# Kernel optimization log

Hardware: AMD Instinct MI355X
Metric: run time of the kernel (lower is better)

The kernel has to match this reference:

```python
import jax, jax.numpy as jnp
import numpy as np

N, E, B = 8192, 131072, 256
F_ATOM, D, H, HD, L, FC, BINS = 92, 256, 8, 32, 6, 512, 256
VMIN, VMAX = 0.0, 8.0


def layer_norm(x, g, b, eps=1e-5):
    mu = jnp.mean(x, axis=-1, keepdims=True)
    var = jnp.var(x, axis=-1, keepdims=True)
    return (x - mu) * jax.lax.rsqrt(var + eps) * g + b


def silu(x):
    return x * jax.nn.sigmoid(x)


def setup_inputs() -> dict:
    key = jax.random.key(0)
    ks = iter(jax.random.split(key, 80))

    def lin(fan_in, shape):
        return jax.random.normal(next(ks), shape, jnp.float32) / np.sqrt(fan_in)

    inp = {
        'x': jax.random.normal(next(ks), (N, F_ATOM), jnp.float32),
        'edge_attr': jax.random.normal(next(ks), (E, 3), jnp.float32) * 2.0,
        'edge_index': jax.random.randint(next(ks), (2, E), 0, N, dtype=jnp.int32),
        'batch': jnp.sort(jax.random.randint(next(ks), (N,), 0, B, dtype=jnp.int32)),
        # atom_embedding: Linear(92,256) -> LN -> SiLU -> Linear(256,256)
        'aw1': lin(F_ATOM, (F_ATOM, D)), 'ab1': jnp.zeros((D,)),
        'ag1': jnp.ones((D,)), 'abt1': jnp.zeros((D,)),
        'aw2': lin(D, (D, D)), 'ab2': jnp.zeros((D,)),
        # rbf MLP: Linear(256,256) LN SiLU Linear LN SiLU Linear
        'rw1': lin(BINS, (BINS, D)), 'rb1': jnp.zeros((D,)),
        'rg1': jnp.ones((D,)), 'rbt1': jnp.zeros((D,)),
        'rw2': lin(D, (D, D)), 'rb2': jnp.zeros((D,)),
        'rg2': jnp.ones((D,)), 'rbt2': jnp.zeros((D,)),
        'rw3': lin(D, (D, D)), 'rb3': jnp.zeros((D,)),
        # L stacked PrdnetConv (edge-conditioned multi-head graph attention)
        'Wq': lin(D, (L, D, D)), 'bq': jnp.zeros((L, D)),
        'Wk': lin(D, (L, D, D)), 'bk': jnp.zeros((L, D)),
        'Wv': lin(D, (L, D, D)), 'bv': jnp.zeros((L, D)),
        'We': lin(D, (L, D, D)), 'be': jnp.zeros((L, D)),
        'Wo': lin(D, (L, D, D)), 'bo': jnp.zeros((L, D)),
        'lng': jnp.ones((L, D)), 'lnb': jnp.zeros((L, D)),
        # FC head: Linear(256,512) then fc_out Linear(512,1)
        'fw1': lin(D, (D, FC)), 'fb1': jnp.zeros((FC,)),
        'fow': lin(FC, (FC, 1)), 'fob': jnp.zeros((1,)),
    }
    return inp


def _forward(x, edge_attr, edge_index, batch, aw1, ab1, ag1, abt1, aw2, ab2,
             rw1, rb1, rg1, rbt1, rw2, rb2, rg2, rbt2, rw3, rb3,
             Wq, bq, Wk, bk, Wv, bv, We, be, Wo, bo, lng, lnb,
             fw1, fb1, fow, fob):
    # atom embedding (dropout = identity at inference)
    node = silu(layer_norm(x @ aw1 + ab1, ag1, abt1)) @ aw2 + ab2  # [N, D]

    # RBF expansion of edge lengths, then edge MLP
    d = jnp.linalg.norm(edge_attr, axis=1)  # [E]
    centers = jnp.linspace(VMIN, VMAX, BINS)
    gamma = 1.0 / (centers[1] - centers[0]) ** 2
    rbf = jnp.exp(-gamma * (d[:, None] - centers[None, :]) ** 2)  # [E, BINS]
    e = silu(layer_norm(rbf @ rw1 + rb1, rg1, rbt1))
    e = silu(layer_norm(e @ rw2 + rb2, rg2, rbt2))
    e = e @ rw3 + rb3  # [E, D]

    src, dst = edge_index[0], edge_index[1]
    inv_sqrt = 1.0 / np.sqrt(HD)
    for l in range(L):
        res = node
        q = (node @ Wq[l] + bq[l]).reshape(N, H, HD)
        k = (node @ Wk[l] + bk[l]).reshape(N, H, HD)
        v = (node @ Wv[l] + bv[l]).reshape(N, H, HD)
        ee = (e @ We[l] + be[l]).reshape(E, H, HD)
        kj = k[src] + ee  # edge-conditioned keys [E, H, HD]
        vj = v[src] + ee  # edge-conditioned values
        score = jnp.sum(q[dst] * kj, axis=-1) * inv_sqrt  # [E, H]
        smax = jax.ops.segment_max(score, dst, num_segments=N)  # [N, H]
        ex = jnp.exp(score - smax[dst])
        den = jax.ops.segment_sum(ex, dst, num_segments=N)
        alpha = ex / (den[dst] + 1e-16)  # neighborhood softmax [E, H]
        msg = jax.ops.segment_sum(alpha[:, :, None] * vj, dst, num_segments=N)
        out = msg.reshape(N, D) @ Wo[l] + bo[l]
        out = layer_norm(out, lng[l], lnb[l])
        node = out + res  # residual

    # scatter-mean graph pooling
    sums = jax.ops.segment_sum(node, batch, num_segments=B)  # [B, D]
    cnt = jax.ops.segment_sum(jnp.ones((N,), node.dtype), batch, num_segments=B)
    feats = sums / jnp.clip(cnt, 1.0)[:, None]

    feats = feats @ fw1 + fb1  # single fc layer: no act (i == len-1 in source)
    return feats @ fow + fob  # [B, 1], identity link


def reference(x, edge_attr, edge_index, batch, aw1, ab1, ag1, abt1, aw2, ab2,
              rw1, rb1, rg1, rbt1, rw2, rb2, rg2, rbt2, rw3, rb3,
              Wq, bq, Wk, bk, Wv, bv, We, be, Wo, bo, lng, lnb,
              fw1, fb1, fow, fob):
    return _forward(x, edge_attr, edge_index, batch, aw1, ab1, ag1, abt1, aw2,
                    ab2, rw1, rb1, rg1, rbt1, rw2, rb2, rg2, rbt2, rw3, rb3,
                    Wq, bq, Wk, bk, Wv, bv, We, be, Wo, bo, lng, lnb,
                    fw1, fb1, fow, fob)
```

## Files before the change

### kernel.cpp

```cpp
#include <hip/hip_runtime.h>
#include <hip/hip_bf16.h>
#include <cstddef>

#define NN    8192
#define EE    131072
#define BB    256
#define F_AT  92
#define DD    256
#define HH    8
#define HDIM  32
#define LL    6
#define FCD   512

typedef __hip_bfloat16 bf16;
typedef __attribute__((ext_vector_type(8))) __bf16 bf16x8;
typedef __attribute__((ext_vector_type(4))) float f32x4;

__device__ __forceinline__ float to_f(float x) { return x; }
__device__ __forceinline__ float to_f(bf16 x) { return __bfloat162float(x); }
__device__ __forceinline__ float bfu(unsigned short u) {
    return __uint_as_float(((unsigned)u) << 16);
}
__device__ __forceinline__ unsigned short bfbits(float x) {
    bf16 h = __float2bfloat16(x);
    return *(unsigned short*)&h;
}
__device__ __forceinline__ void store_v(float* p, float v) { *p = v; }
__device__ __forceinline__ void store_v(bf16* p, float v) { *p = __float2bfloat16(v); }

__device__ __forceinline__ float4 load4(const float* p) { return *(const float4*)p; }
__device__ __forceinline__ float4 load4(const bf16* p) {
    const ushort4 r = *(const ushort4*)p;
    return make_float4(bfu(r.x), bfu(r.y), bfu(r.z), bfu(r.w));
}

__device__ __forceinline__ void store_f4(float* p, const float4& f) {
    *(float4*)p = f;
}
__device__ __forceinline__ void store_f4(bf16* p, const float4& f) {
    ushort4 u = {bfbits(f.x), bfbits(f.y), bfbits(f.z), bfbits(f.w)};
    *(ushort4*)p = u;
}

__device__ __forceinline__ bf16x8 ld8(const bf16* p) { return *(const bf16x8*)p; }
__device__ __forceinline__ bf16x8 ld8(const float* p) {
    const float4 f0 = *(const float4*)p;
    const float4 f1 = *(const float4*)(p + 4);
    bf16x8 r;
    r[0] = (__bf16)f0.x; r[1] = (__bf16)f0.y; r[2] = (__bf16)f0.z; r[3] = (__bf16)f0.w;
    r[4] = (__bf16)f1.x; r[5] = (__bf16)f1.y; r[6] = (__bf16)f1.z; r[7] = (__bf16)f1.w;
    return r;
}

__device__ __forceinline__ void async_copy16(const void* g, void* l) {
    __builtin_amdgcn_global_load_lds(
        (const __attribute__((address_space(1))) unsigned int*)g,
        (__attribute__((address_space(3))) unsigned int*)l, 16, 0, 0);
}

__global__ __launch_bounds__(256) void transpose_weights(
    const float* __restrict__ rw1, const float* __restrict__ rw2,
    const float* __restrict__ rw3, const float* __restrict__ aw2,
    const float* __restrict__ Wq, const float* __restrict__ Wk,
    const float* __restrict__ Wv, const float* __restrict__ We,
    const float* __restrict__ Wo, __bf16* __restrict__ out)
{
    __shared__ float tile[64][65];
    const int midx = blockIdx.y;
    const float* src;
    if (midx == 0) src = rw1;
    else if (midx == 1) src = rw2;
    else if (midx == 2) src = rw3;
    else if (midx == 3) src = aw2;
    else {
        const int l = (midx - 4) / 5, s = (midx - 4) % 5;
        const float* bases[5] = {Wq, Wk, Wv, We, Wo};
        src = bases[s] + (size_t)l * 65536;
    }
    __bf16* dst = out + (size_t)midx * 65536;
    const int k0 = (blockIdx.x >> 2) * 64;
    const int n0 = (blockIdx.x & 3) * 64;
    const int c = threadIdx.x & 63;
    const int r0 = threadIdx.x >> 6;
#pragma unroll
    for (int p = 0; p < 16; ++p) {
        const int r = r0 + p * 4;
        tile[r][c] = src[(size_t)(k0 + r) * 256 + n0 + c];
    }
    __syncthreads();
#pragma unroll
    for (int p = 0; p < 16; ++p) {
        const int n = r0 + p * 4;
        dst[(size_t)(n0 + n) * 256 + k0 + c] = (__bf16)tile[c][n];
    }
}

__global__ __launch_bounds__(256) void pack_qkv_bias(
    const float* __restrict__ bq, const float* __restrict__ bk,
    const float* __restrict__ bv, float* __restrict__ out)
{
    const int i = blockIdx.x * 256 + threadIdx.x;
    if (i >= LL * 768) return;
    const int l = i / 768, r = i % 768;
    const float* s = (r < 256) ? bq : (r < 512) ? bk : bv;
    out[i] = s[l * 256 + (r & 255)];
}

__global__ __launch_bounds__(256) void combine_w3e(
    const float* __restrict__ rw3, const float* __restrict__ We,
    __bf16* __restrict__ Wt_out)
{
    __shared__ float As[16][65];
    __shared__ float Ws[16][65];
    const int l = blockIdx.z;
    const float* W = We + (size_t)l * 65536;
    __bf16* dst = Wt_out + (size_t)l * 65536;
    const int m0 = blockIdx.x * 64;
    const int n0 = blockIdx.y * 64;
    const int tid = threadIdx.x;
    const int tx = tid & 15, ty = tid >> 4;
    float acc[4][4] = {};

    for (int k0 = 0; k0 < 256; k0 += 16) {
        {
            const int ar = tid >> 2;
            const int ac = (tid & 3) * 4;
#pragma unroll
            for (int j = 0; j < 4; ++j)
                As[ac + j][ar] = rw3[(size_t)(m0 + ar) * 256 + k0 + ac + j];
        }
        {
            const int wr = tid >> 4;
            const int wc = (tid & 15) * 4;
#pragma unroll
            for (int j = 0; j < 4; ++j)
                Ws[wr][wc + j] = W[(size_t)(k0 + wr) * 256 + n0 + wc + j];
        }
        __syncthreads();
#pragma unroll
        for (int kk = 0; kk < 16; ++kk) {
            float a[4], b[4];
#pragma unroll
            for (int i = 0; i < 4; ++i) a[i] = As[kk][ty * 4 + i];
#pragma unroll
            for (int j = 0; j < 4; ++j) b[j] = Ws[kk][tx * 4 + j];
#pragma unroll
            for (int i = 0; i < 4; ++i)
#pragma unroll
                for (int j = 0; j < 4; ++j) acc[i][j] += a[i] * b[j];
        }
        __syncthreads();
    }
#pragma unroll
    for (int i = 0; i < 4; ++i) {
        const int gk = m0 + ty * 4 + i;
#pragma unroll
        for (int j = 0; j < 4; ++j) {
            const int gn = n0 + tx * 4 + j;
            dst[(size_t)gn * 256 + gk] = (__bf16)acc[i][j];
        }
    }
}

__global__ __launch_bounds__(256) void combine_bias(
    const float* __restrict__ rb3, const float* __restrict__ We,
    const float* __restrict__ be, float* __restrict__ out)
{
    const int l = blockIdx.x;
    const int n = threadIdx.x;
    const float* W = We + (size_t)l * 65536;
    float s = be[l * 256 + n];
    for (int m = 0; m < 256; ++m) s += rb3[m] * W[m * 256 + n];
    out[l * 256 + n] = s;
}

__global__ __launch_bounds__(256) void mfma_gemm_ln(
    const bf16* __restrict__ A, const __bf16* __restrict__ Wt,
    const float* __restrict__ bias, const float* __restrict__ g,
    const float* __restrict__ b, bf16* __restrict__ C, int do_silu)
{
    __shared__ __align__(16) __bf16 As[64 * 64];
    __shared__ __align__(16) __bf16 Bs[256 * 64];
    const int tid = threadIdx.x;
    const int m0 = blockIdx.x * 64;
    const int wave = tid >> 6, lane = tid & 63;
    const int lm = lane & 15, lq = lane >> 4;
    const int lrow = lane >> 3;
    const int lcolsw = ((lane & 7) ^ lrow) * 8;

    f32x4 acc[16] = {};

    for (int k0 = 0; k0 < 256; k0 += 64) {
#pragma unroll
        for (int p = 0; p < 2; ++p) {
            const int rbase = wave * 16 + p * 8;
            async_copy16(A + (size_t)(m0 + rbase + lrow) * 256 + k0 + lcolsw,
                         As + rbase * 64);
        }
#pragma unroll
        for (int p = 0; p < 8; ++p) {
            const int rbase = wave * 64 + p * 8;
            async_copy16(Wt + (size_t)(rbase + lrow) * 256 + k0 + lcolsw,
                         Bs + rbase * 64);
        }
        __syncthreads();
#pragma unroll
        for (int ks = 0; ks < 2; ++ks) {
            const int sw = ((ks * 4 + lq) ^ (lm & 7)) * 8;
            const bf16x8 a = *(const bf16x8*)(As + (wave * 16 + lm) * 64 + sw);
#pragma unroll
            for (int j = 0; j < 16; ++j) {
                const bf16x8 bf = *(const bf16x8*)(Bs + (j * 16 + lm) * 64 + sw);
                acc[j] = __builtin_amdgcn_mfma_f32_16x16x32_bf16(a, bf, acc[j], 0, 0, 0);
            }
        }
        __syncthreads();
    }

    float gg[16], bb[16];
#pragma unroll
    for (int j = 0; j < 16; ++j) {
        const float bv = bias[j * 16 + lm];
        gg[j] = g[j * 16 + lm];
        bb[j] = b[j * 16 + lm];
#pragma unroll
        for (int r = 0; r < 4; ++r) acc[j][r] += bv;
    }

#pragma unroll
    for (int r = 0; r < 4; ++r) {
        float s = 0.f, q = 0.f;
#pragma unroll
        for (int j = 0; j < 16; ++j) { const float v = acc[j][r]; s += v; q += v * v; }
#pragma unroll
        for (int msk = 1; msk < 16; msk <<= 1) {
            s += __shfl_xor(s, msk);
            q += __shfl_xor(q, msk);
        }
        const float mean = s * (1.f / 256.f);
        const float var = q * (1.f / 256.f) - mean * mean;
        const float rs = rsqrtf(var + 1e-5f);
        bf16* crow = C + (size_t)(m0 + wave * 16 + lq * 4 + r) * 256;
#pragma unroll
        for (int j = 0; j < 16; ++j) {
            float v = (acc[j][r] - mean) * rs * gg[j] + bb[j];
            if (do_silu) v = v / (1.f + __expf(-v));
            crow[j * 16 + lm] = __float2bfloat16(v);
        }
    }
}

template <typename CT>
__global__ __launch_bounds__(256) void mfma_gemm_async(
    const bf16* __restrict__ A, const __bf16* __restrict__ Wt,
    const float* __restrict__ bias, CT* __restrict__ C,
    int M, int Nn, int K)
{
    __shared__ __align__(16) __bf16 As[128 * 64];
    __shared__ __align__(16) __bf16 Bs[128 * 64];
    const int tid = threadIdx.x;
    const int m0 = blockIdx.x * 128;
    const int n0 = blockIdx.y * 128;
    const int wave = tid >> 6, lane = tid & 63;
    const int wm = (wave & 1) * 64, wn = (wave >> 1) * 64;
    const int lm = lane & 15, lq = lane >> 4;
    const int lrow = lane >> 3;
    const int lcolsw = ((lane & 7) ^ lrow) * 8;

    f32x4 acc[4][4] = {};

    for (int k0 = 0; k0 < K; k0 += 64) {
#pragma unroll
        for (int p = 0; p < 4; ++p) {
            const int rbase = wave * 32 + p * 8;
            async_copy16(A  + (size_t)(m0 + rbase + lrow) * K + k0 + lcolsw,
                         As + rbase * 64);
            async_copy16(Wt + (size_t)(n0 + rbase + lrow) * K + k0 + lcolsw,
                         Bs + rbase * 64);
        }
        __syncthreads();
#pragma unroll
        for (int ks = 0; ks < 2; ++ks) {
            const int sw = ((ks * 4 + lq) ^ (lm & 7)) * 8;
            bf16x8 a[4], b[4];
#pragma unroll
            for (int i = 0; i < 4; ++i) {
                a[i] = *(const bf16x8*)(As + (wm + i * 16 + lm) * 64 + sw);
                b[i] = *(const bf16x8*)(Bs + (wn + i * 16 + lm) * 64 + sw);
            }
#pragma unroll
            for (int i = 0; i < 4; ++i)
#pragma unroll
                for (int j = 0; j < 4; ++j)
                    acc[i][j] = __builtin_amdgcn_mfma_f32_16x16x32_bf16(
                        a[i], b[j], acc[i][j], 0, 0, 0);
        }
        __syncthreads();
    }

#pragma unroll
    for (int i = 0; i < 4; ++i) {
        const int gm = m0 + wm + i * 16 + lq * 4;
#pragma unroll
        for (int j = 0; j < 4; ++j) {
            const int gn = n0 + wn + j * 16 + lm;
            const float bv = bias ? bias[gn] : 0.f;
#pragma unroll
            for (int r = 0; r < 4; ++r)
                store_v(&C[(size_t)(gm + r) * Nn + gn], acc[i][j][r] + bv);
        }
    }
}

template <typename AT, typename CT>
__global__ __launch_bounds__(256) void mfma_gemm(
    const AT* __restrict__ A, const __bf16* __restrict__ Wt,
    const float* __restrict__ bias, CT* __restrict__ C,
    int M, int Nn, int K)
{
    __shared__ __align__(16) __bf16 As[128 * 72];
    __shared__ __align__(16) __bf16 Bs[128 * 72];
    const int tid = threadIdx.x;
    const int m0 = blockIdx.x * 128;
    const int n0 = blockIdx.y * 128;
    const int wave = tid >> 6, lane = tid & 63;
    const int wm = (wave & 1) * 64, wn = (wave >> 1) * 64;
    const int lm = lane & 15, lq = lane >> 4;

    f32x4 acc[4][4] = {};

    const int srow = tid >> 3;
    const int scol = (tid & 7) * 8;

    for (int k0 = 0; k0 < K; k0 += 64) {
#pragma unroll
        for (int p = 0; p < 4; ++p) {
            const int r = srow + 32 * p;
            *(bf16x8*)(As + r * 72 + scol) = ld8(A + (size_t)(m0 + r) * K + k0 + scol);
            *(bf16x8*)(Bs + r * 72 + scol) = *(const bf16x8*)(Wt + (size_t)(n0 + r) * K + k0 + scol);
        }
        __syncthreads();
#pragma unroll
        for (int ks = 0; ks < 2; ++ks) {
            bf16x8 a[4], b[4];
#pragma unroll
            for (int i = 0; i < 4; ++i) {
                a[i] = *(const bf16x8*)(As + (wm + i * 16 + lm) * 72 + ks * 32 + lq * 8);
                b[i] = *(const bf16x8*)(Bs + (wn + i * 16 + lm) * 72 + ks * 32 + lq * 8);
            }
#pragma unroll
            for (int i = 0; i < 4; ++i)
#pragma unroll
                for (int j = 0; j < 4; ++j)
                    acc[i][j] = __builtin_amdgcn_mfma_f32_16x16x32_bf16(
                        a[i], b[j], acc[i][j], 0, 0, 0);
        }
        __syncthreads();
    }

#pragma unroll
    for (int i = 0; i < 4; ++i) {
        const int gm = m0 + wm + i * 16 + lq * 4;
#pragma unroll
        for (int j = 0; j < 4; ++j) {
            const int gn = n0 + wn + j * 16 + lm;
            const float bv = bias ? bias[gn] : 0.f;
#pragma unroll
            for (int r = 0; r < 4; ++r)
                store_v(&C[(size_t)(gm + r) * Nn + gn], acc[i][j][r] + bv);
        }
    }
}

template <typename AT, typename CT>
__global__ __launch_bounds__(256) void gemm_bias(
    const AT* __restrict__ A, const float* __restrict__ W,
    const float* __restrict__ bias, CT* __restrict__ C,
    int M, int Nn, int K)
{
    __shared__ float As[16][65];
    __shared__ float Ws[16][65];
    const int m0 = blockIdx.x * 64;
    const int n0 = blockIdx.y * 64;
    const int tid = threadIdx.x;
    const int tx = tid & 15, ty = tid >> 4;
    float acc[4][4] = {};

    for (int k0 = 0; k0 < K; k0 += 16) {
        {
            const int ar = tid >> 2;
            const int ac = (tid & 3) * 4;
            const int gm = m0 + ar;
#pragma unroll
            for (int j = 0; j < 4; ++j) {
                const int gk = k0 + ac + j;
                float v = 0.f;
                if (gm < M && gk < K) v = to_f(A[(size_t)gm * K + gk]);
                As[ac + j][ar] = v;
            }
        }
        {
            const int wr = tid >> 4;
            const int wc = (tid & 15) * 4;
            const int gk = k0 + wr;
#pragma unroll
            for (int j = 0; j < 4; ++j) {
                float v = 0.f;
                if (gk < K) v = W[(size_t)gk * Nn + n0 + wc + j];
                Ws[wr][wc + j] = v;
            }
        }
        __syncthreads();
#pragma unroll
        for (int kk = 0; kk < 16; ++kk) {
            float a[4], b[4];
#pragma unroll
            for (int i = 0; i < 4; ++i) a[i] = As[kk][ty * 4 + i];
#pragma unroll
            for (int j = 0; j < 4; ++j) b[j] = Ws[kk][tx * 4 + j];
#pragma unroll
            for (int i = 0; i < 4; ++i)
#pragma unroll
                for (int j = 0; j < 4; ++j) acc[i][j] += a[i] * b[j];
        }
        __syncthreads();
    }
#pragma unroll
    for (int i = 0; i < 4; ++i) {
        const int gm = m0 + ty * 4 + i;
        if (gm >= M) continue;
#pragma unroll
        for (int j = 0; j < 4; ++j) {
            const int gn = n0 + tx * 4 + j;
            float v = acc[i][j];
            if (bias) v += bias[gn];
            store_v(&C[(size_t)gm * Nn + gn], v);
        }
    }
}

__global__ __launch_bounds__(256) void rbf_kernel(
    const float* __restrict__ ea, const int* __restrict__ eid,
    bf16* __restrict__ rbf)
{
    const int p = blockIdx.x * 4 + (threadIdx.x >> 6);
    const int e = eid[p];
    const int c0 = (threadIdx.x & 63) * 4;
    const float ax = ea[e * 3 + 0];
    const float ay = ea[e * 3 + 1];
    const float az = ea[e * 3 + 2];
    const float d = sqrtf(ax * ax + ay * ay + az * az);
    const float step = 8.0f / 255.0f;
    const float gamma = 1.0f / (step * step);
    float o[4];
#pragma unroll
    for (int j = 0; j < 4; ++j) {
        const float t = d - (float)(c0 + j) * step;
        o[j] = __expf(-gamma * t * t);
    }
    store_f4(rbf + (size_t)p * DD + c0, make_float4(o[0], o[1], o[2], o[3]));
}

template <typename XT, typename YT>
__global__ __launch_bounds__(256) void ln_act_kernel(
    const XT* __restrict__ X, YT* __restrict__ Y,
    const float* __restrict__ g, const float* __restrict__ b,
    const float* __restrict__ resid, int rows, int do_silu)
{
    const int wave = threadIdx.x >> 6;
    const int lane = threadIdx.x & 63;
    const int r = blockIdx.x * 4 + wave;
    if (r >= rows) return;
    const float4 x = load4(X + (size_t)r * DD + lane * 4);
    float s = x.x + x.y + x.z + x.w;
    float q = x.x * x.x + x.y * x.y + x.z * x.z + x.w * x.w;
    for (int off = 32; off; off >>= 1) {
        s += __shfl_down(s, off);
        q += __shfl_down(q, off);
    }
    s = __shfl(s, 0);
    q = __shfl(q, 0);
    const float mean = s * (1.f / 256.f);
    const float var = q * (1.f / 256.f) - mean * mean;
    const float rs = rsqrtf(var + 1e-5f);
    const int c = lane * 4;
    float xs[4] = {x.x, x.y, x.z, x.w};
    float out[4];
#pragma unroll
    for (int i = 0; i < 4; ++i) {
        float v = (xs[i] - mean) * rs * g[c + i] + b[c + i];
        if (do_silu) v = v / (1.f + __expf(-v));
        out[i] = v;
    }
    if (resid) {
        const float4 rv = load4(resid + (size_t)r * DD + c);
        out[0] += rv.x; out[1] += rv.y; out[2] += rv.z; out[3] += rv.w;
    }
    store_f4(Y + (size_t)r * DD + c, make_float4(out[0], out[1], out[2], out[3]));
}

__global__ __launch_bounds__(256) void deg_kernel(
    const int* __restrict__ dst, int* __restrict__ deg)
{
    const int e = blockIdx.x * 256 + threadIdx.x;
    if (e < EE) atomicAdd(&deg[dst[e]], 1);
}

__global__ __launch_bounds__(256) void csr_scan(
    const int* __restrict__ deg, int* __restrict__ rowptr)
{
    __shared__ int part[256];
    const int t = threadIdx.x;
    int local[32];
    int s = 0;
#pragma unroll
    for (int i = 0; i < 32; ++i) { local[i] = deg[t * 32 + i]; s += local[i]; }
    part[t] = s;
    __syncthreads();
    if (t == 0) {
        int run = 0;
        for (int i = 0; i < 256; ++i) { const int v = part[i]; part[i] = run; run += v; }
    }
    __syncthreads();
    int run = part[t];
#pragma unroll
    for (int i = 0; i < 32; ++i) { rowptr[t * 32 + i] = run; run += local[i]; }
    if (t == 255) rowptr[NN] = run;
}

__global__ __launch_bounds__(256) void fill_kernel(
    const int* __restrict__ src, const int* __restrict__ dst,
    const int* __restrict__ rowptr, int* __restrict__ fill,
    int* __restrict__ eid, int* __restrict__ srcc)
{
    const int e = blockIdx.x * 256 + threadIdx.x;
    if (e >= EE) return;
    const int d = dst[e];
    const int pos = atomicAdd(&fill[d], 1);
    const int q = rowptr[d] + pos;
    eid[q] = e;
    srcc[q] = src[e];
}

__global__ __launch_bounds__(256) void attn_kernel(
    const bf16* __restrict__ qkv, const bf16* __restrict__ ee, int estride,
    const int* __restrict__ rowptr, const int* __restrict__ srcc,
    float* __restrict__ msg)
{
    const int n = blockIdx.x;
    const int tid = threadIdx.x;
    const int wave = tid >> 6, lane = tid & 63;
    const int e0 = rowptr[n];
    const int deg = rowptr[n + 1] - e0;

    if (deg == 0) {
        msg[(size_t)n * DD + tid] = 0.f;
        return;
    }

    __shared__ float wm[4][HH];
    __shared__ float wl[4][HH];
    __shared__ float wacc[4][DD];

    const float4 qreg = load4(qkv + (size_t)n * 768 + lane * 4);

    float m = -3.402823466e38f, l = 0.f;
    float4 acc = {0.f, 0.f, 0.f, 0.f};

    for (int j = wave; j < deg; j += 4) {
        const int e = e0 + j;
        const int s_ = srcc[e];
        const bf16* srow = qkv + (size_t)s_ * 768;
        const float4 kv = load4(srow + 256 + lane * 4);
        const float4 vv = load4(srow + 512 + lane * 4);
        const float4 ev = load4(ee + (size_t)e * estride + lane * 4);
        float p = qreg.x * (kv.x + ev.x) + qreg.y * (kv.y + ev.y) +
                  qreg.z * (kv.z + ev.z) + qreg.w * (kv.w + ev.w);
        p += __shfl_down(p, 4);
        p += __shfl_down(p, 2);
        p += __shfl_down(p, 1);
        const float s = __shfl(p, lane & 56) * 0.17677669529663687f;
        const float mnew = fmaxf(m, s);
        const float scale = __expf(m - mnew);
        const float pe = __expf(s - mnew);
        l = l * scale + pe;
        acc.x = acc.x * scale + pe * (vv.x + ev.x);
        acc.y = acc.y * scale + pe * (vv.y + ev.y);
        acc.z = acc.z * scale + pe * (vv.z + ev.z);
        acc.w = acc.w * scale + pe * (vv.w + ev.w);
        m = mnew;
    }

    if ((lane & 7) == 0) { wm[wave][lane >> 3] = m; wl[wave][lane >> 3] = l; }
    *(float4*)(&wacc[wave][lane * 4]) = acc;
    __syncthreads();

    {
        const int c = tid, h = tid >> 5;
        float M = wm[0][h];
#pragma unroll
        for (int i = 1; i < 4; ++i) M = fmaxf(M, wm[i][h]);
        float L = 0.f, num = 0.f;
#pragma unroll
        for (int i = 0; i < 4; ++i) {
            const float sc = __expf(wm[i][h] - M);
            L += wl[i][h] * sc;
            num += wacc[i][c] * sc;
        }
        msg[(size_t)n * DD + c] = num / (L + 1e-16f);
    }
}

__global__ __launch_bounds__(256) void zero_kernel(float* __restrict__ p, int n)
{
    const int i = blockIdx.x * 256 + threadIdx.x;
    if (i < n) p[i] = 0.f;
}

__global__ __launch_bounds__(256) void pool_kernel(
    const float* __restrict__ node, const int* __restrict__ batch,
    float* __restrict__ sums, float* __restrict__ cnt)
{
    const int n = blockIdx.x;
    const int c = threadIdx.x;
    const int b = batch[n];
    atomicAdd(&sums[b * DD + c], node[(size_t)n * DD + c]);
    if (c == 0) atomicAdd(&cnt[b], 1.0f);
}

__global__ __launch_bounds__(256) void pooled_kernel(
    const float* __restrict__ sums, const float* __restrict__ cnt,
    float* __restrict__ pooled)
{
    const int b = blockIdx.x;
    const int c = threadIdx.x;
    float cc = cnt[b];
    if (cc < 1.f) cc = 1.f;
    pooled[b * DD + c] = sums[b * DD + c] / cc;
}

__global__ __launch_bounds__(64) void final_kernel(
    const float* __restrict__ fc, const float* __restrict__ fow,
    const float* __restrict__ fob, float* __restrict__ out)
{
    const int b = blockIdx.x;
    const int lane = threadIdx.x;
    float s = 0.f;
#pragma unroll
    for (int i = lane; i < FCD; i += 64) s += fc[(size_t)b * FCD + i] * fow[i];
    for (int off = 32; off; off >>= 1) s += __shfl_down(s, off);
    if (lane == 0) out[b] = s + fob[0];
}

extern "C" void kernel_launch(void* const* d_in, const int* in_sizes, int n_in,
                              void* d_out, int out_size, void* d_ws,
                              size_t ws_size, hipStream_t stream)
{
    const float* x         = (const float*)d_in[0];
    const float* edge_attr = (const float*)d_in[1];
    const int*   eidx      = (const int*)d_in[2];
    const int*   batch     = (const int*)d_in[3];
    const float* aw1 = (const float*)d_in[4];
    const float* ab1 = (const float*)d_in[5];
    const float* ag1 = (const float*)d_in[6];
    const float* abt1 = (const float*)d_in[7];
    const float* aw2 = (const float*)d_in[8];
    const float* ab2 = (const float*)d_in[9];
    const float* rw1 = (const float*)d_in[10];
    const float* rb1 = (const float*)d_in[11];
    const float* rg1 = (const float*)d_in[12];
    const float* rbt1 = (const float*)d_in[13];
    const float* rw2 = (const float*)d_in[14];
    const float* rb2 = (const float*)d_in[15];
    const float* rg2 = (const float*)d_in[16];
    const float* rbt2 = (const float*)d_in[17];
    const float* rw3 = (const float*)d_in[18];
    const float* rb3 = (const float*)d_in[19];
    const float* Wq = (const float*)d_in[20];
    const float* bq = (const float*)d_in[21];
    const float* Wk = (const float*)d_in[22];
    const float* bk = (const float*)d_in[23];
    const float* Wv = (const float*)d_in[24];
    const float* bv = (const float*)d_in[25];
    const float* We_ = (const float*)d_in[26];
    const float* be_ = (const float*)d_in[27];
    const float* Wo = (const float*)d_in[28];
    const float* bo = (const float*)d_in[29];
    const float* lng = (const float*)d_in[30];
    const float* lnb = (const float*)d_in[31];
    const float* fw1 = (const float*)d_in[32];
    const float* fb1 = (const float*)d_in[33];
    const float* fow = (const float*)d_in[34];
    const float* fob = (const float*)d_in[35];

    const int* src = eidx;
    const int* dst = eidx + EE;

    char* w = (char*)d_ws;
    size_t off = 0;
    auto alloc = [&](size_t bytes) -> void* {
        void* p = w + off;
        off += (bytes + 255) & ~(size_t)255;
        return p;
    };
    bf16* t_buf = (bf16*)alloc((size_t)EE * DD * 2);
    float* node = (float*)alloc((size_t)NN * DD * 4);
    bf16*  qkv  = (bf16*)alloc((size_t)NN * 768 * 2);
    float* msg  = (float*)alloc((size_t)NN * DD * 4);
    float* outb = (float*)alloc((size_t)NN * DD * 4);
    int* deg    = (int*)alloc((size_t)NN * 4);
    int* fillc  = (int*)alloc((size_t)NN * 4);
    int* rowptr = (int*)alloc((size_t)(NN + 1) * 4);
    int* eid    = (int*)alloc((size_t)EE * 4);
    int* srcc   = (int*)alloc((size_t)EE * 4);
    float* sums  = (float*)alloc((size_t)BB * DD * 4);
    float* cnt   = (float*)alloc((size_t)BB * 4);
    float* pooled = (float*)alloc((size_t)BB * DD * 4);
    float* fc    = (float*)alloc((size_t)BB * FCD * 4);
    __bf16* Wt  = (__bf16*)alloc((size_t)40 * 65536 * 2);
    float* qkvb = (float*)alloc((size_t)LL * 768 * 4);
    float* be_c = (float*)alloc((size_t)LL * 256 * 4);

    const size_t avail = (off <= ws_size) ? ws_size - off : 0;
    int G = 1;
    if      (avail >= (size_t)EE * (6 * DD) * 2 + 256) G = 6;
    else if (avail >= (size_t)EE * (3 * DD) * 2 + 256) G = 3;
    else if (avail >= (size_t)EE * (2 * DD) * 2 + 256) G = 2;
    bf16* e_slab = (bf16*)alloc((size_t)EE * (G * DD) * 2);
    (void)n_in; (void)in_sizes; (void)out_size;

    const dim3 blk(256);
    auto WT = [&](int i) -> const __bf16* { return Wt + (size_t)i * 65536; };

    hipLaunchKernelGGL(transpose_weights, dim3(16, 34), blk, 0, stream,
                       rw1, rw2, rw3, aw2, Wq, Wk, Wv, We_, Wo, Wt);
    hipLaunchKernelGGL(combine_w3e, dim3(4, 4, LL), blk, 0, stream, rw3, We_, Wt + (size_t)34 * 65536);
    hipLaunchKernelGGL(combine_bias, dim3(LL), blk, 0, stream, rb3, We_, be_, be_c);
    hipLaunchKernelGGL(pack_qkv_bias, dim3((LL * 768 + 255) / 256), blk, 0, stream, bq, bk, bv, qkvb);
    hipLaunchKernelGGL(zero_kernel, dim3((2 * NN + 255) / 256), blk, 0, stream, (float*)deg, 2 * NN);
    hipLaunchKernelGGL(deg_kernel, dim3(EE / 256), blk, 0, stream, dst, deg);
    hipLaunchKernelGGL(csr_scan, dim3(1), blk, 0, stream, deg, rowptr);
    hipLaunchKernelGGL(fill_kernel, dim3(EE / 256), blk, 0, stream, src, dst, rowptr, fillc, eid, srcc);

    hipLaunchKernelGGL(rbf_kernel, dim3(EE / 4), blk, 0, stream, edge_attr, eid, t_buf);
    hipLaunchKernelGGL(mfma_gemm_ln, dim3(EE / 64), blk, 0, stream, t_buf, WT(0), rb1, rg1, rbt1, e_slab, 1);
    hipLaunchKernelGGL(mfma_gemm_ln, dim3(EE / 64), blk, 0, stream, e_slab, WT(1), rb2, rg2, rbt2, t_buf, 1);

    {
        dim3 gn64(NN / 64, DD / 64);
        hipLaunchKernelGGL((gemm_bias<float, float>), gn64, blk, 0, stream, x, aw1, ab1, outb, NN, DD, F_AT);
        hipLaunchKernelGGL((ln_act_kernel<float, float>), dim3(NN / 4), blk, 0, stream, outb, outb, ag1, abt1, (const float*)nullptr, NN, 1);
        hipLaunchKernelGGL((mfma_gemm<float, float>), dim3(NN / 128, DD / 128), blk, 0, stream, outb, WT(3), ab2, node, NN, DD, DD);
    }

    for (int l = 0; l < LL; ++l) {
        const size_t bo_ = (size_t)l * DD;
        hipLaunchKernelGGL((mfma_gemm<float, bf16>), dim3(NN / 128, 768 / 128), blk, 0, stream,
                           node, WT(4 + 5 * l), qkvb + (size_t)l * 768, qkv, NN, 768, DD);
        if (l % G == 0) {
            hipLaunchKernelGGL((mfma_gemm_async<bf16>), dim3(EE / 128, (G * DD) / 128), blk, 0, stream,
                               t_buf, WT(34 + l), be_c + (size_t)l * 256, e_slab, EE, G * DD, DD);
        }
        const bf16* ee_l = e_slab + (size_t)(l % G) * DD;
        hipLaunchKernelGGL(attn_kernel, dim3(NN), blk, 0, stream, qkv, ee_l, G * DD, rowptr, srcc, msg);
        hipLaunchKernelGGL((mfma_gemm<float, float>), dim3(NN / 128, DD / 128), blk, 0, stream, msg, WT(8 + 5 * l), bo + bo_, outb, NN, DD, DD);
        hipLaunchKernelGGL((ln_act_kernel<float, float>), dim3(NN / 4), blk, 0, stream, outb, node, lng + bo_, lnb + bo_, node, NN, 0);
    }

    const int PZ = BB * DD + BB;
    hipLaunchKernelGGL(zero_kernel, dim3((PZ + 255) / 256), blk, 0, stream, sums, PZ);
    hipLaunchKernelGGL(pool_kernel, dim3(NN), blk, 0, stream, node, batch, sums, cnt);
    hipLaunchKernelGGL(pooled_kernel, dim3(BB), blk, 0, stream, sums, cnt, pooled);
    {
        dim3 gf(BB / 64, FCD / 64);
        hipLaunchKernelGGL((gemm_bias<float, float>), gf, blk, 0, stream, pooled, fw1, fb1, fc, BB, FCD, DD);
    }
    hipLaunchKernelGGL(final_kernel, dim3(BB), dim3(64), 0, stream, fc, fow, fob, (float*)d_out);
}
```

Measured before the change: 1.034 ms.

## Prefetch next edge's K/V/E in attention loop and swap edge GEMM grid order

The attention kernel's per-wave edge loop now software-pipelines its gathers, loading the next edge's key, value and edge rows while the current edge is processed. This is meant to hide gather latency behind the online-softmax math, at the cost of extra registers. Separately, the edge-feature GEMM grid is transposed so that blocks sharing the same A row tile run back to back across the N tiles. This should improve L2 reuse of the large edge activation matrix.

```diff
diff --git a/kernel.cpp b/kernel.cpp
--- a/kernel.cpp
+++ b/kernel.cpp
@@ -259,8 +259,8 @@
     __shared__ __align__(16) __bf16 As[128 * 64];
     __shared__ __align__(16) __bf16 Bs[128 * 64];
     const int tid = threadIdx.x;
-    const int m0 = blockIdx.x * 128;
-    const int n0 = blockIdx.y * 128;
+    const int m0 = blockIdx.y * 128;
+    const int n0 = blockIdx.x * 128;
     const int wave = tid >> 6, lane = tid & 63;
     const int wm = (wave & 1) * 64, wn = (wave >> 1) * 64;
     const int lm = lane & 15, lq = lane >> 4;
@@ -567,13 +567,27 @@
     float m = -3.402823466e38f, l = 0.f;
     float4 acc = {0.f, 0.f, 0.f, 0.f};
 
-    for (int j = wave; j < deg; j += 4) {
+    int j = wave;
+    float4 kv = {0.f, 0.f, 0.f, 0.f};
+    float4 vv = kv, ev = kv;
+    if (j < deg) {
         const int e = e0 + j;
-        const int s_ = srcc[e];
-        const bf16* srow = qkv + (size_t)s_ * 768;
-        const float4 kv = load4(srow + 256 + lane * 4);
-        const float4 vv = load4(srow + 512 + lane * 4);
-        const float4 ev = load4(ee + (size_t)e * estride + lane * 4);
+        const bf16* srow = qkv + (size_t)srcc[e] * 768;
+        kv = load4(srow + 256 + lane * 4);
+        vv = load4(srow + 512 + lane * 4);
+        ev = load4(ee + (size_t)e * estride + lane * 4);
+    }
+    while (j < deg) {
+        const int jn = j + 4;
+        float4 kv2 = {0.f, 0.f, 0.f, 0.f};
+        float4 vv2 = kv2, ev2 = kv2;
+        if (jn < deg) {
+            const int e2 = e0 + jn;
+            const bf16* srow2 = qkv + (size_t)srcc[e2] * 768;
+            kv2 = load4(srow2 + 256 + lane * 4);
+            vv2 = load4(srow2 + 512 + lane * 4);
+            ev2 = load4(ee + (size_t)e2 * estride + lane * 4);
+        }
         float p = qreg.x * (kv.x + ev.x) + qreg.y * (kv.y + ev.y) +
                   qreg.z * (kv.z + ev.z) + qreg.w * (kv.w + ev.w);
         p += __shfl_down(p, 4);
@@ -589,6 +603,8 @@
         acc.z = acc.z * scale + pe * (vv.z + ev.z);
         acc.w = acc.w * scale + pe * (vv.w + ev.w);
         m = mnew;
+        kv = kv2; vv = vv2; ev = ev2;
+        j = jn;
     }
 
     if ((lane & 7) == 0) { wm[wave][lane >> 3] = m; wl[wave][lane >> 3] = l; }
@@ -758,7 +774,7 @@
         hipLaunchKernelGGL((mfma_gemm<float, bf16>), dim3(NN / 128, 768 / 128), blk, 0, stream,
                            node, WT(4 + 5 * l), qkvb + (size_t)l * 768, qkv, NN, 768, DD);
         if (l % G == 0) {
-            hipLaunchKernelGGL((mfma_gemm_async<bf16>), dim3(EE / 128, (G * DD) / 128), blk, 0, stream,
+            hipLaunchKernelGGL((mfma_gemm_async<bf16>), dim3((G * DD) / 128, EE / 128), blk, 0, stream,
                                t_buf, WT(34 + l), be_c + (size_t)l * 256, e_slab, EE, G * DD, DD);
         }
         const bf16* ee_l = e_slab + (size_t)(l % G) * DD;
```

Result: faster. 1.001 ms (-3.3%).

## Prefetch attention edges two-deep and add XCD-aware tiling with staged stores to edge GEMM

Applied to the files above, without the earlier changes.

The attention kernel now keeps two independent online-softmax streams per wave and issues the gathers for the next pair of edges before computing the current pair, so more loads are in flight to hide gather latency. The two streams are merged at the end. The edge GEMM uses a 1D grid remapped so each XCD gets a contiguous block of M tiles, which should improve L2 locality. It also stages its output through shared memory to write 16-byte coalesced rows instead of scattered scalar bf16 stores. The cost is higher register pressure in the attention kernel, plus an extra LDS round trip and barrier in the GEMM epilogue.

```diff
diff --git a/kernel.cpp b/kernel.cpp
--- a/kernel.cpp
+++ b/kernel.cpp
@@ -250,17 +250,23 @@
     }
 }
 
-template <typename CT>
-__global__ __launch_bounds__(256) void mfma_gemm_async(
+__global__ __launch_bounds__(256) void mfma_gemm_ee(
     const bf16* __restrict__ A, const __bf16* __restrict__ Wt,
-    const float* __restrict__ bias, CT* __restrict__ C,
+    const float* __restrict__ bias, bf16* __restrict__ C,
     int M, int Nn, int K)
 {
-    __shared__ __align__(16) __bf16 As[128 * 64];
-    __shared__ __align__(16) __bf16 Bs[128 * 64];
+    __shared__ __align__(16) __bf16 smem[128 * 128];
+    __bf16* As = smem;
+    __bf16* Bs = smem + 128 * 64;
     const int tid = threadIdx.x;
-    const int m0 = blockIdx.x * 128;
-    const int n0 = blockIdx.y * 128;
+
+    const int nt_n = Nn >> 7;
+    const int xcd = blockIdx.x & 7;
+    const int local = blockIdx.x >> 3;
+    const int per_xcd = (M >> 7) >> 3;
+    const int m0 = (xcd * per_xcd + local / nt_n) * 128;
+    const int n0 = (local % nt_n) * 128;
+
     const int wave = tid >> 6, lane = tid & 63;
     const int wm = (wave & 1) * 64, wn = (wave >> 1) * 64;
     const int lm = lane & 15, lq = lane >> 4;
@@ -300,15 +306,24 @@
 
 #pragma unroll
     for (int i = 0; i < 4; ++i) {
-        const int gm = m0 + wm + i * 16 + lq * 4;
+        const int rl = wm + i * 16 + lq * 4;
 #pragma unroll
         for (int j = 0; j < 4; ++j) {
-            const int gn = n0 + wn + j * 16 + lm;
-            const float bv = bias ? bias[gn] : 0.f;
+            const int cl = wn + j * 16 + lm;
+            const float bb = bias ? bias[n0 + cl] : 0.f;
 #pragma unroll
             for (int r = 0; r < 4; ++r)
-                store_v(&C[(size_t)(gm + r) * Nn + gn], acc[i][j][r] + bv);
-        }
+                smem[(rl + r) * 128 + cl] = (__bf16)(acc[i][j][r] + bb);
+        }
+    }
+    __syncthreads();
+#pragma unroll
+    for (int p = 0; p < 8; ++p) {
+        const int ch = tid + p * 256;
+        const int row = ch >> 4;
+        const int col = (ch & 15) * 8;
+        *(bf16x8*)((__bf16*)C + (size_t)(m0 + row) * Nn + n0 + col) =
+            *(const bf16x8*)(smem + row * 128 + col);
     }
 }
 
@@ -564,34 +579,101 @@
 
     const float4 qreg = load4(qkv + (size_t)n * 768 + lane * 4);
 
-    float m = -3.402823466e38f, l = 0.f;
-    float4 acc = {0.f, 0.f, 0.f, 0.f};
-
-    for (int j = wave; j < deg; j += 4) {
+    float mA = -3.402823466e38f, lA = 0.f;
+    float mB = -3.402823466e38f, lB = 0.f;
+    float4 accA = {0.f, 0.f, 0.f, 0.f};
+    float4 accB = {0.f, 0.f, 0.f, 0.f};
+
+    const float4 z4 = {0.f, 0.f, 0.f, 0.f};
+    int j = wave;
+    float4 kvA = z4, vvA = z4, evA = z4;
+    float4 kvB = z4, vvB = z4, evB = z4;
+    bool hasA = (j < deg), hasB = (j + 4 < deg);
+    if (hasA) {
         const int e = e0 + j;
-        const int s_ = srcc[e];
-        const bf16* srow = qkv + (size_t)s_ * 768;
-        const float4 kv = load4(srow + 256 + lane * 4);
-        const float4 vv = load4(srow + 512 + lane * 4);
-        const float4 ev = load4(ee + (size_t)e * estride + lane * 4);
-        float p = qreg.x * (kv.x + ev.x) + qreg.y * (kv.y + ev.y) +
-                  qreg.z * (kv.z + ev.z) + qreg.w * (kv.w + ev.w);
-        p += __shfl_down(p, 4);
-        p += __shfl_down(p, 2);
-        p += __shfl_down(p, 1);
-        const float s = __shfl(p, lane & 56) * 0.17677669529663687f;
-        const float mnew = fmaxf(m, s);
-        const float scale = __expf(m - mnew);
-        const float pe = __expf(s - mnew);
-        l = l * scale + pe;
-        acc.x = acc.x * scale + pe * (vv.x + ev.x);
-        acc.y = acc.y * scale + pe * (vv.y + ev.y);
-        acc.z = acc.z * scale + pe * (vv.z + ev.z);
-        acc.w = acc.w * scale + pe * (vv.w + ev.w);
-        m = mnew;
-    }
-
-    if ((lane & 7) == 0) { wm[wave][lane >> 3] = m; wl[wave][lane >> 3] = l; }
+        const bf16* srow = qkv + (size_t)srcc[e] * 768;
+        kvA = load4(srow + 256 + lane * 4);
+        vvA = load4(srow + 512 + lane * 4);
+        evA = load4(ee + (size_t)e * estride + lane * 4);
+    }
+    if (hasB) {
+        const int e = e0 + j + 4;
+        const bf16* srow = qkv + (size_t)srcc[e] * 768;
+        kvB = load4(srow + 256 + lane * 4);
+        vvB = load4(srow + 512 + lane * 4);
+        evB = load4(ee + (size_t)e * estride + lane * 4);
+    }
+
+    while (hasA) {
+        const int jn = j + 8;
+        float4 kv2A = z4, vv2A = z4, ev2A = z4;
+        float4 kv2B = z4, vv2B = z4, ev2B = z4;
+        const bool nA = (jn < deg), nB = (jn + 4 < deg);
+        if (nA) {
+            const int e = e0 + jn;
+            const bf16* srow = qkv + (size_t)srcc[e] * 768;
+            kv2A = load4(srow + 256 + lane * 4);
+            vv2A = load4(srow + 512 + lane * 4);
+            ev2A = load4(ee + (size_t)e * estride + lane * 4);
+        }
+        if (nB) {
+            const int e = e0 + jn + 4;
+            const bf16* srow = qkv + (size_t)srcc[e] * 768;
+            kv2B = load4(srow + 256 + lane * 4);
+            vv2B = load4(srow + 512 + lane * 4);
+            ev2B = load4(ee + (size_t)e * estride + lane * 4);
+        }
+
+        {
+            float p = qreg.x * (kvA.x + evA.x) + qreg.y * (kvA.y + evA.y) +
+                      qreg.z * (kvA.z + evA.z) + qreg.w * (kvA.w + evA.w);
+            p += __shfl_down(p, 4);
+            p += __shfl_down(p, 2);
+            p += __shfl_down(p, 1);
+            const float s = __shfl(p, lane & 56) * 0.17677669529663687f;
+            const float mnew = fmaxf(mA, s);
+            const float scale = __expf(mA - mnew);
+            const float pe = __expf(s - mnew);
+            lA = lA * scale + pe;
+            accA.x = accA.x * scale + pe * (vvA.x + evA.x);
+            accA.y = accA.y * scale + pe * (vvA.y + evA.y);
+            accA.z = accA.z * scale + pe * (vvA.z + evA.z);
+            accA.w = accA.w * scale + pe * (vvA.w + evA.w);
+            mA = mnew;
+        }
+        if (hasB) {
+            float p = qreg.x * (kvB.x + evB.x) + qreg.y * (kvB.y + evB.y) +
+                      qreg.z * (kvB.z + evB.z) + qreg.w * (kvB.w + evB.w);
+            p += __shfl_down(p, 4);
+            p += __shfl_down(p, 2);
+            p += __shfl_down(p, 1);
+            const float s = __shfl(p, lane & 56) * 0.17677669529663687f;
+            const float mnew = fmaxf(mB, s);
+            const float scale = __expf(mB - mnew);
+            const float pe = __expf(s - mnew);
+            lB = lB * scale + pe;
+            accB.x = accB.x * scale + pe * (vvB.x + evB.x);
+            accB.y = accB.y * scale + pe * (vvB.y + evB.y);
+            accB.z = accB.z * scale + pe * (vvB.z + evB.z);
+            accB.w = accB.w * scale + pe * (vvB.w + evB.w);
+            mB = mnew;
+        }
+        kvA = kv2A; vvA = vv2A; evA = ev2A;
+        kvB = kv2B; vvB = vv2B; evB = ev2B;
+        hasA = nA; hasB = nB;
+        j = jn;
+    }
+
+    const float mm = fmaxf(mA, mB);
+    const float sA = __expf(mA - mm), sB = __expf(mB - mm);
+    const float l = lA * sA + lB * sB;
+    float4 acc;
+    acc.x = accA.x * sA + accB.x * sB;
+    acc.y = accA.y * sA + accB.y * sB;
+    acc.z = accA.z * sA + accB.z * sB;
+    acc.w = accA.w * sA + accB.w * sB;
+
+    if ((lane & 7) == 0) { wm[wave][lane >> 3] = mm; wl[wave][lane >> 3] = l; }
     *(float4*)(&wacc[wave][lane * 4]) = acc;
     __syncthreads();
 
@@ -758,7 +840,8 @@
         hipLaunchKernelGGL((mfma_gemm<float, bf16>), dim3(NN / 128, 768 / 128), blk, 0, stream,
                            node, WT(4 + 5 * l), qkvb + (size_t)l * 768, qkv, NN, 768, DD);
         if (l % G == 0) {
-            hipLaunchKernelGGL((mfma_gemm_async<bf16>), dim3(EE / 128, (G * DD) / 128), blk, 0, stream,
+            const int nblocks = (EE / 128) * ((G * DD) / 128);
+            hipLaunchKernelGGL(mfma_gemm_ee, dim3(nblocks), blk, 0, stream,
                                t_buf, WT(34 + l), be_c + (size_t)l * 256, e_slab, EE, G * DD, DD);
         }
         const bf16* ee_l = e_slab + (size_t)(l % G) * DD;
```

Result: no change. 1.048 ms (+1.4%).
